# Optimization experiments

Measured on AMD Instinct MI355X. Metric: run time of the kernel, lower is better.

The kernel has to match this reference:

```python
import jax, jax.numpy as jnp
import numpy as np

B, T, D, H, HS = 2, 256, 2048, 32, 64
LORA, DLORA, ST = 32, 64, 66  # maa lora rank, decay lora rank, state rows (2+HS)
EPS = 1e-5


def setup_inputs() -> dict:
    key = jax.random.key(0)
    ks = jax.random.split(key, 24)
    n = lambda k, sh, s=0.02: (jax.random.normal(k, sh, jnp.float32) * s)
    u = lambda k, sh: jax.random.uniform(k, sh, jnp.float32)
    return {
        "x": jax.random.normal(ks[0], (B, T, D), jnp.float32),
        "state": jax.random.normal(ks[1], (B, ST, D), jnp.float32) * 0.1,
        "ln1_w": jnp.ones((D,), jnp.float32),
        "ln1_b": jnp.zeros((D,), jnp.float32),
        "time_maa_x": u(ks[2], (D,)),
        "time_maa_w1": n(ks[3], (D, 5 * LORA)),
        "time_maa_w2": n(ks[4], (5, LORA, D)),
        "time_maa_k": u(ks[5], (D,)),
        "time_maa_w": u(ks[6], (D,)),
        "time_maa_v": u(ks[7], (D,)),
        "time_maa_r": u(ks[8], (D,)),
        "time_maa_g": u(ks[9], (D,)),
        "time_decay": n(ks[10], (D,), 0.5),
        "time_decay_w1": n(ks[11], (D, DLORA)),
        "time_decay_w2": n(ks[12], (DLORA, D)),
        "time_faaaa": n(ks[13], (H, HS, 1), 0.1),
        "receptance_weight": n(ks[14], (D, D)),
        "key_weight": n(ks[15], (D, D)),
        "value_weight": n(ks[16], (D, D)),
        "output_weight": n(ks[17], (D, D)),
        "gate_weight": n(ks[18], (D, D)),
        "lnx_w": jnp.ones((D,), jnp.float32),
        "lnx_b": jnp.zeros((D,), jnp.float32),
        "i": 0,
    }


def reference(x, state, ln1_w, ln1_b, time_maa_x, time_maa_w1, time_maa_w2,
              time_maa_k, time_maa_w, time_maa_v, time_maa_r, time_maa_g,
              time_decay, time_decay_w1, time_decay_w2, time_faaaa,
              receptance_weight, key_weight, value_weight, output_weight,
              gate_weight, lnx_w, lnx_b, i):
    # forward() early-returns time_mixing(ln1(x), state, i)
    mu = x.mean(-1, keepdims=True)
    var = ((x - mu) ** 2).mean(-1, keepdims=True)
    x = (x - mu) * jax.lax.rsqrt(var + EPS) * ln1_w + ln1_b

    i1 = (2 + HS) * i + 1
    # token shift: sx[t] = x[t-1] - x[t], with state row i1 as x[-1]
    sx = jnp.concatenate([state[:, i1][:, None] - x[:, :1], x[:, :-1] - x[:, 1:]], axis=1)

    xxx = x + sx * time_maa_x
    t5 = jnp.tanh(xxx @ time_maa_w1).reshape(B, T, 5, LORA)
    xxx5 = jnp.einsum('btfr,frd->btfd', t5, time_maa_w2)          # [B,T,5,D]
    maa = jnp.stack([time_maa_k, time_maa_w, time_maa_v, time_maa_r, time_maa_g])  # [5,D]
    x5 = x[:, :, None] + sx[:, :, None] * (maa + xxx5)            # [B,T,5,D]

    k = (x5[:, :, 0] @ key_weight.T).reshape(B, T, H, HS)
    w = jnp.exp(-jnp.exp(time_decay + jnp.tanh(x5[:, :, 1] @ time_decay_w1) @ time_decay_w2)).reshape(B, T, H, HS)
    v = (x5[:, :, 2] @ value_weight.T).reshape(B, T, H, HS)
    r = (x5[:, :, 3] @ receptance_weight.T).reshape(B, T, H, HS)
    g = jax.nn.silu(x5[:, :, 4] @ gate_weight.T)                  # [B,T,D]

    kv = jnp.einsum('bthi,bthj->bthij', k, v)                     # [B,T,H,HS,HS]
    prev0 = state[:, i1 + 1:i1 + 1 + HS].reshape(B, H, HS, HS)

    def step(prev, xs):
        kv_t, w_t = xs
        return kv_t + w_t[..., None] * prev, prev  # emit state BEFORE update

    _, state_s = jax.lax.scan(step, prev0,
                              (kv.transpose(1, 0, 2, 3, 4), w.transpose(1, 0, 2, 3)))
    state_s = state_s.transpose(1, 0, 2, 3, 4)                    # [B,T,H,HS,HS]

    wkv = time_faaaa * kv + state_s
    rwkv = jnp.einsum('bthj,bthjd->bthd', r, wkv)                 # [B,T,H,HS]

    # GroupNorm(num_groups=H) over each head's HS channels
    gm = rwkv.mean(-1, keepdims=True)
    gv = ((rwkv - gm) ** 2).mean(-1, keepdims=True)
    normed = (rwkv - gm) * jax.lax.rsqrt(gv + EPS)
    normed = normed * lnx_w.reshape(H, HS) + lnx_b.reshape(H, HS)
    normed = normed.reshape(B, T, D)

    return (normed * g) @ output_weight.T
```

## Files before the change

kernel.cpp:

```cpp
#include <hip/hip_runtime.h>
#include <hip/hip_bf16.h>

typedef unsigned short u16;
typedef __attribute__((ext_vector_type(4))) float f32x4;
typedef __attribute__((ext_vector_type(8))) short short8;
typedef __attribute__((ext_vector_type(4))) short bf16x4;

#define B_ 2
#define T_ 256
#define D_ 2048
#define H_ 32
#define HS_ 64
#define M_ 512
#define ST_ 66
#define EPS_ 1e-5f

__device__ __forceinline__ float bf2f(u16 u) {
    union { unsigned int i; float f; } c; c.i = ((unsigned int)u) << 16; return c.f;
}
__device__ __forceinline__ u16 f2bf(float f) {
    union { unsigned int i; float f; } c; c.f = f;
    unsigned int r = c.i + 0x7fffu + ((c.i >> 16) & 1u);
    return (u16)(r >> 16);
}

__device__ __forceinline__ void gld16(const u16* g, u16* l) {
    __builtin_amdgcn_global_load_lds((const __attribute__((address_space(1))) void*)g,
                                     (__attribute__((address_space(3))) void*)l, 16, 0, 0);
}

__global__ __launch_bounds__(256) void wcvt_kernel(const float* __restrict__ wk, const float* __restrict__ wv,
                                                   const float* __restrict__ wr, const float* __restrict__ wg,
                                                   const float* __restrict__ wo, u16* __restrict__ out)
{
    const int wsel = blockIdx.y;
    const float* in = (wsel == 0) ? wk : (wsel == 1) ? wv : (wsel == 2) ? wr : (wsel == 3) ? wg : wo;
    const size_t e = ((size_t)blockIdx.x * 256 + threadIdx.x) * 8;
    f32x4 a = *(const f32x4*)(in + e);
    f32x4 b = *(const f32x4*)(in + e + 4);
    short8 o;
#pragma unroll
    for (int i = 0; i < 4; i++) { o[i] = (short)f2bf(a[i]); o[i + 4] = (short)f2bf(b[i]); }
    *(short8*)(out + (size_t)wsel * D_ * D_ + e) = o;
}

__global__ __launch_bounds__(256) void ln_kernel(const float* __restrict__ x, const float* __restrict__ w,
                                                 const float* __restrict__ bias, float* __restrict__ xln)
{
    const int row = blockIdx.x;
    const float* xr = x + (size_t)row * D_;
    float* orow = xln + (size_t)row * D_;
    const int t = threadIdx.x;
    f32x4 a0 = *(const f32x4*)(xr + t * 8);
    f32x4 a1 = *(const f32x4*)(xr + t * 8 + 4);
    float s = 0.f, q = 0.f;
#pragma unroll
    for (int i = 0; i < 4; i++) { s += a0[i] + a1[i]; q += a0[i]*a0[i] + a1[i]*a1[i]; }
#pragma unroll
    for (int off = 1; off < 64; off <<= 1) { s += __shfl_xor(s, off, 64); q += __shfl_xor(q, off, 64); }
    __shared__ float ls[4], lq[4];
    const int wid = t >> 6, lane = t & 63;
    if (lane == 0) { ls[wid] = s; lq[wid] = q; }
    __syncthreads();
    s = ls[0] + ls[1] + ls[2] + ls[3];
    q = lq[0] + lq[1] + lq[2] + lq[3];
    const float mu = s * (1.f / D_);
    const float var = q * (1.f / D_) - mu * mu;
    const float rs = rsqrtf(var + EPS_);
#pragma unroll
    for (int i = 0; i < 8; i++) {
        int d = t * 8 + i;
        float f = (i < 4) ? a0[i] : a1[i - 4];
        orow[d] = (f - mu) * rs * w[d] + bias[d];
    }
}

__global__ __launch_bounds__(256) void shift_kernel(const float* __restrict__ xln, const float* __restrict__ state,
                                                    const float* __restrict__ maax, const int* __restrict__ ip,
                                                    float* __restrict__ sx, u16* __restrict__ xxxb)
{
    const size_t gid = (size_t)blockIdx.x * 256 + threadIdx.x;
    const size_t e = gid * 4;
    const int row = (int)(e >> 11);
    const int d = (int)(e & 2047);
    const int tt = row & (T_ - 1);
    const int b = row >> 8;
    const float* prev;
    if (tt == 0) prev = state + ((size_t)b * ST_ + (size_t)(66 * ip[0] + 1)) * D_ + d;
    else         prev = xln + e - D_;
    f32x4 p = *(const f32x4*)prev;
    f32x4 c = *(const f32x4*)(xln + e);
    f32x4 mx = *(const f32x4*)(maax + d);
    f32x4 sv;
    bf16x4 xv;
#pragma unroll
    for (int i = 0; i < 4; i++) { sv[i] = p[i] - c[i]; xv[i] = (short)f2bf(c[i] + sv[i] * mx[i]); }
    *(f32x4*)(sx + e) = sv;
    *(bf16x4*)(xxxb + e) = xv;
}

__global__ __launch_bounds__(256) void txp_kernel(const float* __restrict__ in, u16* __restrict__ out,
                                                  int K, int N)
{
    __shared__ float tile[32][33];
    const int k0 = blockIdx.x * 32, n0 = blockIdx.y * 32;
    const int c = threadIdx.x & 31, r8 = threadIdx.x >> 5;
#pragma unroll
    for (int i = 0; i < 4; i++) {
        int r = r8 + i * 8;
        tile[r][c] = in[(size_t)(k0 + r) * N + (n0 + c)];
    }
    __syncthreads();
#pragma unroll
    for (int i = 0; i < 4; i++) {
        int r = r8 + i * 8;
        out[(size_t)(n0 + r) * K + (k0 + c)] = f2bf(tile[c][r]);
    }
}

template<int NN, bool TANH>
__global__ __launch_bounds__(256) void gsmall_kernel(const u16* __restrict__ A, const u16* __restrict__ Wt,
                                                     float* __restrict__ C, int ldc)
{
    __shared__ u16 As[128 * 32];
    __shared__ u16 Ws[64 * 32];
    const int tid = threadIdx.x;
    const int m0 = blockIdx.y * 128, n0 = blockIdx.x * 64;
    const int lane = tid & 63, wid = tid >> 6;
    const int wm = (wid >> 1) * 64, wn = (wid & 1) * 32;

    f32x4 acc[4][2];
#pragma unroll
    for (int i = 0; i < 4; i++)
#pragma unroll
        for (int j = 0; j < 2; j++) { acc[i][j][0]=0.f; acc[i][j][1]=0.f; acc[i][j][2]=0.f; acc[i][j][3]=0.f; }

    const int rA = tid >> 2;
    const int kA = (tid & 3) * 8;
    const u16* gA0 = A + (size_t)(m0 + rA) * D_ + kA;
    const u16* gA1 = A + (size_t)(m0 + rA + 64) * D_ + kA;
    int wrow = n0 + rA; if (wrow >= NN) wrow = NN - 1;
    const u16* gW = Wt + (size_t)wrow * D_ + kA;
    u16* lA0 = As + tid * 8;
    u16* lA1 = As + (tid + 256) * 8;
    u16* lW  = Ws + tid * 8;
    const u16* pa = As + (size_t)(wm + (lane & 15)) * 32 + (lane >> 4) * 8;
    const u16* pb = Ws + (size_t)(wn + (lane & 15)) * 32 + (lane >> 4) * 8;

    short8 a0 = *(const short8*)gA0;
    short8 a1 = *(const short8*)gA1;
    short8 w0 = *(const short8*)gW;

    for (int kt = 0; kt < D_; kt += 32) {
        const int kt2 = (kt + 32) & (D_ - 1);
        short8 na0 = *(const short8*)(gA0 + kt2);
        short8 na1 = *(const short8*)(gA1 + kt2);
        short8 nw0 = *(const short8*)(gW + kt2);
        __syncthreads();
        *(short8*)lA0 = a0;
        *(short8*)lA1 = a1;
        *(short8*)lW  = w0;
        __syncthreads();
        short8 av[4], bv[2];
#pragma unroll
        for (int mi = 0; mi < 4; mi++) av[mi] = *(const short8*)(pa + mi * 16 * 32);
#pragma unroll
        for (int ni = 0; ni < 2; ni++) bv[ni] = *(const short8*)(pb + ni * 16 * 32);
#pragma unroll
        for (int mi = 0; mi < 4; mi++)
#pragma unroll
            for (int ni = 0; ni < 2; ni++)
                acc[mi][ni] = __builtin_amdgcn_mfma_f32_16x16x32_bf16(av[mi], bv[ni], acc[mi][ni], 0, 0, 0);
        a0 = na0; a1 = na1; w0 = nw0;
    }
    const int cr = wm + (lane >> 4) * 4;
    const int cc = wn + (lane & 15);
#pragma unroll
    for (int mi = 0; mi < 4; mi++)
#pragma unroll
        for (int ni = 0; ni < 2; ni++) {
            const int col = n0 + cc + ni * 16;
            if (col < NN) {
#pragma unroll
                for (int j = 0; j < 4; j++) {
                    float v = acc[mi][ni][j];
                    if (TANH) v = tanhf(v);
                    C[(size_t)(m0 + cr + mi * 16 + j) * ldc + col] = v;
                }
            }
        }
}

__global__ __launch_bounds__(256) void maa2_kernel(const float* __restrict__ t5, const float* __restrict__ w2,
                                                   const float* __restrict__ xln, const float* __restrict__ sxp,
                                                   const float* __restrict__ mk, const float* __restrict__ mw,
                                                   const float* __restrict__ mv, const float* __restrict__ mr,
                                                   const float* __restrict__ mg, u16* __restrict__ x5)
{
    const int gid = blockIdx.x * 256 + threadIdx.x;
    const int d = gid & (D_ - 1);
    const int f = (gid >> 11) % 5;
    const int mg4 = gid / (5 * D_);
    const float* maa = (f == 0) ? mk : (f == 1) ? mw : (f == 2) ? mv : (f == 3) ? mr : mg;
    const float mf = maa[d];
    const float* w2f = w2 + (size_t)f * 32 * D_ + d;
    const float* t5b = t5 + (size_t)mg4 * 4 * 160 + f * 32;
    float a0 = 0, a1 = 0, a2 = 0, a3 = 0;
#pragma unroll 8
    for (int r = 0; r < 32; r++) {
        float wv = w2f[(size_t)r * D_];
        a0 = fmaf(t5b[r], wv, a0);
        a1 = fmaf(t5b[160 + r], wv, a1);
        a2 = fmaf(t5b[320 + r], wv, a2);
        a3 = fmaf(t5b[480 + r], wv, a3);
    }
    const float accs[4] = {a0, a1, a2, a3};
    const size_t m0 = (size_t)mg4 * 4;
#pragma unroll
    for (int mm = 0; mm < 4; mm++) {
        size_t e = (m0 + mm) * D_ + d;
        x5[(size_t)f * M_ * D_ + e] = f2bf(xln[e] + sxp[e] * (mf + accs[mm]));
    }
}

__global__ __launch_bounds__(256) void decay2_kernel(const float* __restrict__ td, const float* __restrict__ dw2,
                                                     const float* __restrict__ tdec, float* __restrict__ wout)
{
    const int gid = blockIdx.x * 256 + threadIdx.x;
    const int d = gid & (D_ - 1);
    const int mg4 = gid >> 11;
    const float* wp = dw2 + d;
    const float* tb = td + (size_t)mg4 * 4 * 64;
    float a0 = 0, a1 = 0, a2 = 0, a3 = 0;
#pragma unroll 8
    for (int r = 0; r < 64; r++) {
        float wv = wp[(size_t)r * D_];
        a0 = fmaf(tb[r], wv, a0);
        a1 = fmaf(tb[64 + r], wv, a1);
        a2 = fmaf(tb[128 + r], wv, a2);
        a3 = fmaf(tb[192 + r], wv, a3);
    }
    const float base = tdec[d];
    const float accs[4] = {a0, a1, a2, a3};
#pragma unroll
    for (int mm = 0; mm < 4; mm++)
        wout[((size_t)mg4 * 4 + mm) * D_ + d] = expf(-expf(base + accs[mm]));
}

__device__ __forceinline__ void gemm2p_body(const u16* __restrict__ A, const u16* __restrict__ Wb,
                                            float* __restrict__ C, int m0, int n0, int k0, int KC)
{
    __shared__ u16 As[2][128 * 64];
    __shared__ u16 Bs[2][64 * 64];
    const int tid = threadIdx.x;
    const int lane = tid & 63;
    const int wvd = tid >> 6;
    const int wm = (wvd >> 1) * 64;
    const int wn = (wvd & 1) * 32;

    f32x4 acc[4][2];
#pragma unroll
    for (int i = 0; i < 4; i++)
#pragma unroll
        for (int j = 0; j < 2; j++) { acc[i][j][0]=0.f; acc[i][j][1]=0.f; acc[i][j][2]=0.f; acc[i][j][3]=0.f; }

    const int srow = tid >> 3;
    const int sw8  = (((tid & 7) ^ (srow & 7)) << 3);
    const u16* Ag = A + (size_t)(m0 + srow) * D_ + k0 + sw8;
    const u16* Wg = Wb + (size_t)(n0 + srow) * D_ + k0 + sw8;
    const int ldst = tid * 8;

    const int rsw = (lane & 7) << 3;
    const int colb = (lane >> 4) * 8;
    const int fr = lane & 15;

#define STAGE_(bb, kt)                                                            \
    {                                                                             \
        _Pragma("unroll")                                                         \
        for (int i = 0; i < 4; i++)                                               \
            gld16(Ag + (size_t)(i * 32) * D_ + (kt), &As[bb][i * 2048 + ldst]);   \
        _Pragma("unroll")                                                         \
        for (int i = 0; i < 2; i++)                                               \
            gld16(Wg + (size_t)(i * 32) * D_ + (kt), &Bs[bb][i * 2048 + ldst]);   \
    }

    STAGE_(0, 0);
    __syncthreads();
    int cur = 0;
    for (int kt = 0; kt < KC; kt += 64) {
        if (kt + 64 < KC) STAGE_(cur ^ 1, kt + 64);
#pragma unroll
        for (int kk = 0; kk < 64; kk += 32) {
            const int c = (kk + colb) ^ rsw;
            short8 av[4], bv[2];
#pragma unroll
            for (int mi = 0; mi < 4; mi++)
                av[mi] = *(const short8*)&As[cur][(wm + mi * 16 + fr) * 64 + c];
#pragma unroll
            for (int ni = 0; ni < 2; ni++)
                bv[ni] = *(const short8*)&Bs[cur][(wn + ni * 16 + fr) * 64 + c];
#pragma unroll
            for (int mi = 0; mi < 4; mi++)
#pragma unroll
                for (int ni = 0; ni < 2; ni++)
                    acc[mi][ni] = __builtin_amdgcn_mfma_f32_16x16x32_bf16(av[mi], bv[ni], acc[mi][ni], 0, 0, 0);
        }
        __syncthreads();
        cur ^= 1;
    }
#undef STAGE_
    const int cr = wm + (lane >> 4) * 4;
    const int cc = wn + fr;
#pragma unroll
    for (int mi = 0; mi < 4; mi++)
#pragma unroll
        for (int ni = 0; ni < 2; ni++)
#pragma unroll
            for (int j = 0; j < 4; j++)
                C[(size_t)(m0 + cr + mi * 16 + j) * D_ + (n0 + cc + ni * 16)] = acc[mi][ni][j];
}

__global__ __launch_bounds__(256) void gemm4g_kernel(const u16* __restrict__ x5, const u16* __restrict__ wcvt,
                                                     float* __restrict__ kvK, float* __restrict__ kvV,
                                                     float* __restrict__ kvR, float* __restrict__ kvG)
{
    const int s = blockIdx.z;
    const u16* A = x5 + (size_t)(s == 0 ? 0 : s + 1) * M_ * D_;
    const u16* W = wcvt + (size_t)s * D_ * D_;
    float* C = (s == 0) ? kvK : (s == 1) ? kvV : (s == 2) ? kvR : kvG;
    gemm2p_body(A, W, C, blockIdx.y * 128, blockIdx.x * 64, 0, D_);
}

__global__ __launch_bounds__(256) void gemm1g_kernel(const u16* __restrict__ y, const u16* __restrict__ wo,
                                                     float* __restrict__ out, float* __restrict__ p0,
                                                     float* __restrict__ p1, float* __restrict__ p2)
{
    const int ks = blockIdx.z;
    float* C = (ks == 0) ? out : (ks == 1) ? p0 : (ks == 2) ? p1 : p2;
    gemm2p_body(y, wo, C, blockIdx.y * 128, blockIdx.x * 64, ks * 512, 512);
}

__global__ __launch_bounds__(256) void add3_kernel(float* __restrict__ dst, const float* __restrict__ s0,
                                                   const float* __restrict__ s1, const float* __restrict__ s2)
{
    const size_t e = ((size_t)blockIdx.x * 256 + threadIdx.x) * 4;
    f32x4 d = *(const f32x4*)(dst + e);
    f32x4 a = *(const f32x4*)(s0 + e);
    f32x4 b = *(const f32x4*)(s1 + e);
    f32x4 c = *(const f32x4*)(s2 + e);
#pragma unroll
    for (int i = 0; i < 4; i++) d[i] += (a[i] + b[i]) + c[i];
    *(f32x4*)(dst + e) = d;
}

#define CH_ 16
__global__ __launch_bounds__(512) void rec_kernel(const float* __restrict__ rB, const float* __restrict__ kB,
                                                  const float* __restrict__ wB, const float* __restrict__ vB,
                                                  const float* __restrict__ fa, const float* __restrict__ state,
                                                  const int* __restrict__ ip, float* __restrict__ rwkv)
{
    const int bh = blockIdx.x;
    const int b = bh >> 5, h = bh & 31;
    const int tid = threadIdx.x;
    const int wv = tid >> 6, lane = tid & 63;
    const int wg = wv >> 2;
    const int jb = lane >> 3, dsub = lane & 7;
    const int jbase = jb * 8;
    const int d0 = wg * 32 + (wv & 3) * 8 + dsub;

    __shared__ float stage[2][4][CH_][64];
    __shared__ float p2[CH_][8][64];
    __shared__ float p1[CH_][8];

    float S[8], faj[8];
    {
        const float* Sp = state + (size_t)b * ST_ * D_ + (size_t)(66 * ip[0] + 2) * D_ + (size_t)h * HS_ * HS_;
#pragma unroll
        for (int jj = 0; jj < 8; jj++) {
            S[jj]   = Sp[(jbase + jj) * 64 + d0];
            faj[jj] = fa[h * 64 + jbase + jj];
        }
    }
    const size_t base = ((size_t)b * T_ * H_ + h) * HS_;
    const int arr = wv & 3;
    const float* mysrc = (arr == 0) ? rB : (arr == 1) ? kB : (arr == 2) ? wB : vB;
    const int ts0 = wg * 8 + (lane >> 4);
    const int sch = (lane & 15) * 4;
    const bool p1w = (wv == 0 && dsub == 0);

    f32x4 pre[2];
#pragma unroll
    for (int p = 0; p < 2; p++)
        pre[p] = *(const f32x4*)(mysrc + base + (size_t)(ts0 + p * 4) * (H_ * HS_) + sch);
#pragma unroll
    for (int p = 0; p < 2; p++)
        *(f32x4*)&stage[0][arr][ts0 + p * 4][sch] = pre[p];
    __syncthreads();

    int cb = 0;
    for (int c = 0; c < T_ / CH_; ++c) {
        const bool more = (c + 1 < T_ / CH_);
        if (more) {
#pragma unroll
            for (int p = 0; p < 2; p++)
                pre[p] = *(const f32x4*)(mysrc + base + (size_t)((c + 1) * CH_ + ts0 + p * 4) * (H_ * HS_) + sch);
        }
        f32x4 r0 = *(const f32x4*)&stage[cb][0][0][jbase];
        f32x4 r1 = *(const f32x4*)&stage[cb][0][0][jbase + 4];
        f32x4 k0 = *(const f32x4*)&stage[cb][1][0][jbase];
        f32x4 k1 = *(const f32x4*)&stage[cb][1][0][jbase + 4];
        f32x4 w0 = *(const f32x4*)&stage[cb][2][0][jbase];
        f32x4 w1 = *(const f32x4*)&stage[cb][2][0][jbase + 4];
        float vd = stage[cb][3][0][d0];
#pragma unroll
        for (int ts = 0; ts < CH_; ++ts) {
            f32x4 nr0 = r0, nr1 = r1, nk0 = k0, nk1 = k1, nw0 = w0, nw1 = w1;
            float nvd = vd;
            if (ts + 1 < CH_) {
                nr0 = *(const f32x4*)&stage[cb][0][ts + 1][jbase];
                nr1 = *(const f32x4*)&stage[cb][0][ts + 1][jbase + 4];
                nk0 = *(const f32x4*)&stage[cb][1][ts + 1][jbase];
                nk1 = *(const f32x4*)&stage[cb][1][ts + 1][jbase + 4];
                nw0 = *(const f32x4*)&stage[cb][2][ts + 1][jbase];
                nw1 = *(const f32x4*)&stage[cb][2][ts + 1][jbase + 4];
                nvd = stage[cb][3][ts + 1][d0];
            }
            float s1 = 0.f, s2 = 0.f;
#pragma unroll
            for (int q = 0; q < 4; q++) {
                s1 = fmaf(r0[q] * faj[q],     k0[q], s1);
                s1 = fmaf(r1[q] * faj[q + 4], k1[q], s1);
                s2 = fmaf(r0[q], S[q],     s2);
                s2 = fmaf(r1[q], S[q + 4], s2);
            }
            p2[ts][jb][d0 ^ (jb << 3)] = s2;
            if (p1w) p1[ts][jb] = s1;
#pragma unroll
            for (int q = 0; q < 4; q++) {
                S[q]     = fmaf(w0[q], S[q],     k0[q] * vd);
                S[q + 4] = fmaf(w1[q], S[q + 4], k1[q] * vd);
            }
            r0 = nr0; r1 = nr1; k0 = nk0; k1 = nk1; w0 = nw0; w1 = nw1; vd = nvd;
        }
        if (more) {
#pragma unroll
            for (int p = 0; p < 2; p++)
                *(f32x4*)&stage[cb ^ 1][arr][ts0 + p * 4][sch] = pre[p];
        }
        __syncthreads();
#pragma unroll
        for (int p = 0; p < 2; p++) {
            const int ts = wv * 2 + p;
            f32x4 p1a = *(const f32x4*)&p1[ts][0];
            f32x4 p1b = *(const f32x4*)&p1[ts][4];
            float s1t = ((p1a[0] + p1a[1]) + (p1a[2] + p1a[3])) +
                        ((p1b[0] + p1b[1]) + (p1b[2] + p1b[3]));
            float s2t = 0.f;
#pragma unroll
            for (int j = 0; j < 8; j++) s2t += p2[ts][j][lane ^ (j << 3)];
            const float vvv = stage[cb][3][ts][lane];
            rwkv[base + (size_t)(c * CH_ + ts) * (H_ * HS_) + lane] = fmaf(vvv, s1t, s2t);
        }
        __syncthreads();
        cb ^= 1;
    }
}

__global__ __launch_bounds__(256) void gn_kernel(const float* __restrict__ rwkv, const float* __restrict__ gpre,
                                                 const float* __restrict__ lnxw, const float* __restrict__ lnxb,
                                                 u16* __restrict__ y)
{
    const int g = blockIdx.x * 4 + (threadIdx.x >> 6);
    const int lane = threadIdx.x & 63;
    const size_t e = (size_t)g * 64 + lane;
    const float val = rwkv[e];
    float s = val, q = val * val;
#pragma unroll
    for (int off = 1; off < 64; off <<= 1) { s += __shfl_xor(s, off, 64); q += __shfl_xor(q, off, 64); }
    const float mu = s * (1.f / 64.f);
    const float var = q * (1.f / 64.f) - mu * mu;
    const float rs = rsqrtf(var + EPS_);
    const int hj = (int)(e & (size_t)(D_ - 1));
    const float nrm = (val - mu) * rs * lnxw[hj] + lnxb[hj];
    const float gp = gpre[e];
    const float gv = gp / (1.f + expf(-gp));
    y[e] = f2bf(nrm * gv);
}

extern "C" void kernel_launch(void* const* d_in, const int* in_sizes, int n_in,
                              void* d_out, int out_size, void* d_ws, size_t ws_size,
                              hipStream_t stream)
{
    const float* x     = (const float*)d_in[0];
    const float* state = (const float*)d_in[1];
    const float* ln1w  = (const float*)d_in[2];
    const float* ln1b  = (const float*)d_in[3];
    const float* maax  = (const float*)d_in[4];
    const float* w1    = (const float*)d_in[5];
    const float* w2    = (const float*)d_in[6];
    const float* maak  = (const float*)d_in[7];
    const float* maaw  = (const float*)d_in[8];
    const float* maav  = (const float*)d_in[9];
    const float* maar  = (const float*)d_in[10];
    const float* maag  = (const float*)d_in[11];
    const float* tdec  = (const float*)d_in[12];
    const float* dw1   = (const float*)d_in[13];
    const float* dw2   = (const float*)d_in[14];
    const float* fa    = (const float*)d_in[15];
    const float* wrec  = (const float*)d_in[16];
    const float* wkey  = (const float*)d_in[17];
    const float* wval  = (const float*)d_in[18];
    const float* wout  = (const float*)d_in[19];
    const float* wgate = (const float*)d_in[20];
    const float* lnxw  = (const float*)d_in[21];
    const float* lnxb  = (const float*)d_in[22];
    const int*   ip    = (const int*)d_in[23];

    char* ws = (char*)d_ws;
    const size_t MD = (size_t)M_ * D_;
    u16*   wcvt = (u16*)  (ws);
    float* xln  = (float*)(ws + ((size_t)40 << 20));
    float* sx   = (float*)(ws + ((size_t)44 << 20));
    u16*   xxxb = (u16*)  (ws + ((size_t)48 << 20));
    u16*   w1t  = (u16*)  (ws + ((size_t)50 << 20));
    u16*   dw1t = (u16*)  (ws + ((size_t)51 << 20));
    float* t5   = (float*)(ws + ((size_t)52 << 20));
    float* td   = (float*)(ws + ((size_t)53 << 20));
    u16*   x5   = (u16*)  (ws + ((size_t)54 << 20));
    float* wdec = (float*)(ws + ((size_t)64 << 20));
    float* kvK  = (float*)(ws + ((size_t)40 << 20));
    float* kvV  = (float*)(ws + ((size_t)44 << 20));
    float* kvR  = (float*)(ws + ((size_t)48 << 20));
    float* kvG  = (float*)(ws + ((size_t)68 << 20));
    float* rwkv = (float*)(ws + ((size_t)72 << 20));
    u16*   y    = (u16*)  (ws + ((size_t)76 << 20));
    float* pp0  = (float*)(ws + ((size_t)54 << 20));
    float* pp1  = (float*)(ws + ((size_t)58 << 20));
    float* pp2  = (float*)(ws + ((size_t)62 << 20));
    float* out  = (float*)d_out;

    hipLaunchKernelGGL(wcvt_kernel,   dim3(2048, 5),  dim3(256), 0, stream, wkey, wval, wrec, wgate, wout, wcvt);
    hipLaunchKernelGGL(ln_kernel,     dim3(512),      dim3(256), 0, stream, x, ln1w, ln1b, xln);
    hipLaunchKernelGGL(shift_kernel,  dim3(1024),     dim3(256), 0, stream, xln, state, maax, ip, sx, xxxb);
    hipLaunchKernelGGL(txp_kernel,    dim3(64, 5),    dim3(256), 0, stream, w1, w1t, D_, 160);
    hipLaunchKernelGGL(txp_kernel,    dim3(64, 2),    dim3(256), 0, stream, dw1, dw1t, D_, 64);
    hipLaunchKernelGGL((gsmall_kernel<160, true>), dim3(3, 4), dim3(256), 0, stream, xxxb, w1t, t5, 160);
    hipLaunchKernelGGL(maa2_kernel,   dim3(5120),     dim3(256), 0, stream, t5, w2, xln, sx, maak, maaw, maav, maar, maag, x5);
    hipLaunchKernelGGL((gsmall_kernel<64, true>),  dim3(1, 4), dim3(256), 0, stream, x5 + MD, dw1t, td, 64);
    hipLaunchKernelGGL(decay2_kernel, dim3(1024),     dim3(256), 0, stream, td, dw2, tdec, wdec);
    hipLaunchKernelGGL(gemm4g_kernel, dim3(32, 4, 4), dim3(256), 0, stream, x5, wcvt, kvK, kvV, kvR, kvG);
    hipLaunchKernelGGL(rec_kernel,    dim3(64),       dim3(512), 0, stream, kvR, kvK, wdec, kvV, fa, state, ip, rwkv);
    hipLaunchKernelGGL(gn_kernel,     dim3(4096),     dim3(256), 0, stream, rwkv, kvG, lnxw, lnxb, y);
    hipLaunchKernelGGL(gemm1g_kernel, dim3(32, 4, 4), dim3(256), 0, stream, y, wcvt + (size_t)4 * D_ * D_, out, pp0, pp1, pp2);
    hipLaunchKernelGGL(add3_kernel,   dim3(1024),     dim3(256), 0, stream, out, pp0, pp1, pp2);

    (void)in_sizes; (void)n_in; (void)out_size; (void)ws_size;
}
```

Baseline: 213.8 us.

## Split WKV recurrence into chunked parallel scan across blocks

Replaces the single sequential recurrence kernel (64 blocks iterating all 256 timesteps) with a three-phase chunked scan. Chunks run in parallel from zero state while recording decay products. A small pass then propagates carry states across chunks, and a final pass adds the carried-state contribution via r·prod(w) times the chunk start state. This exposes 16x more blocks to use the GPU, at the cost of two extra launches and extra global traffic for per-chunk states. Workspace at offset 0 is reused for chunk states, which overlaps the weight-conversion buffer.

```diff
diff --git a/kernel.cpp b/kernel.cpp
--- a/kernel.cpp
+++ b/kernel.cpp
@@ -14,6 +14,8 @@
 #define M_ 512
 #define ST_ 66
 #define EPS_ 1e-5f
+#define NC_ 16
+#define CL_ 16
 
 __device__ __forceinline__ float bf2f(u16 u) {
     union { unsigned int i; float f; } c; c.i = ((unsigned int)u) << 16; return c.f;
@@ -353,14 +355,16 @@
     *(f32x4*)(dst + e) = d;
 }
 
-#define CH_ 16
-__global__ __launch_bounds__(512) void rec_kernel(const float* __restrict__ rB, const float* __restrict__ kB,
-                                                  const float* __restrict__ wB, const float* __restrict__ vB,
-                                                  const float* __restrict__ fa, const float* __restrict__ state,
-                                                  const int* __restrict__ ip, float* __restrict__ rwkv)
-{
-    const int bh = blockIdx.x;
-    const int b = bh >> 5, h = bh & 31;
+__global__ __launch_bounds__(512) void rec1_kernel(const float* __restrict__ rB, const float* __restrict__ kB,
+                                                   const float* __restrict__ wB, const float* __restrict__ vB,
+                                                   const float* __restrict__ fa, float* __restrict__ rwkv,
+                                                   float* __restrict__ CS, float* __restrict__ RP,
+                                                   float* __restrict__ PC)
+{
+    const int bx = blockIdx.x;
+    const int c  = bx & (NC_ - 1);
+    const int bh = bx >> 4;
+    const int h = bh & 31, b = bh >> 5;
     const int tid = threadIdx.x;
     const int wv = tid >> 6, lane = tid & 63;
     const int wg = wv >> 2;
@@ -368,102 +372,159 @@
     const int jbase = jb * 8;
     const int d0 = wg * 32 + (wv & 3) * 8 + dsub;
 
-    __shared__ float stage[2][4][CH_][64];
-    __shared__ float p2[CH_][8][64];
-    __shared__ float p1[CH_][8];
-
-    float S[8], faj[8];
-    {
-        const float* Sp = state + (size_t)b * ST_ * D_ + (size_t)(66 * ip[0] + 2) * D_ + (size_t)h * HS_ * HS_;
-#pragma unroll
-        for (int jj = 0; jj < 8; jj++) {
-            S[jj]   = Sp[(jbase + jj) * 64 + d0];
-            faj[jj] = fa[h * 64 + jbase + jj];
-        }
-    }
+    __shared__ float stage[4][CL_][64];
+    __shared__ float p2[CL_][8][64];
+    __shared__ float p1[CL_][8];
+    __shared__ float rpS[CL_ * 64];
+
+    float S[8], pv[8], faj[8];
+#pragma unroll
+    for (int q = 0; q < 8; q++) { S[q] = 0.f; pv[q] = 1.f; faj[q] = fa[h * 64 + jbase + q]; }
+
     const size_t base = ((size_t)b * T_ * H_ + h) * HS_;
+    const int t0 = c * CL_;
     const int arr = wv & 3;
     const float* mysrc = (arr == 0) ? rB : (arr == 1) ? kB : (arr == 2) ? wB : vB;
     const int ts0 = wg * 8 + (lane >> 4);
     const int sch = (lane & 15) * 4;
     const bool p1w = (wv == 0 && dsub == 0);
 
-    f32x4 pre[2];
-#pragma unroll
-    for (int p = 0; p < 2; p++)
-        pre[p] = *(const f32x4*)(mysrc + base + (size_t)(ts0 + p * 4) * (H_ * HS_) + sch);
-#pragma unroll
-    for (int p = 0; p < 2; p++)
-        *(f32x4*)&stage[0][arr][ts0 + p * 4][sch] = pre[p];
+#pragma unroll
+    for (int p = 0; p < 2; p++) {
+        f32x4 v = *(const f32x4*)(mysrc + base + (size_t)(t0 + ts0 + p * 4) * (H_ * HS_) + sch);
+        *(f32x4*)&stage[arr][ts0 + p * 4][sch] = v;
+    }
     __syncthreads();
 
-    int cb = 0;
-    for (int c = 0; c < T_ / CH_; ++c) {
-        const bool more = (c + 1 < T_ / CH_);
-        if (more) {
-#pragma unroll
-            for (int p = 0; p < 2; p++)
-                pre[p] = *(const f32x4*)(mysrc + base + (size_t)((c + 1) * CH_ + ts0 + p * 4) * (H_ * HS_) + sch);
+    f32x4 r0 = *(const f32x4*)&stage[0][0][jbase];
+    f32x4 r1 = *(const f32x4*)&stage[0][0][jbase + 4];
+    f32x4 k0 = *(const f32x4*)&stage[1][0][jbase];
+    f32x4 k1 = *(const f32x4*)&stage[1][0][jbase + 4];
+    f32x4 w0 = *(const f32x4*)&stage[2][0][jbase];
+    f32x4 w1 = *(const f32x4*)&stage[2][0][jbase + 4];
+    float vd = stage[3][0][d0];
+#pragma unroll
+    for (int ts = 0; ts < CL_; ++ts) {
+        f32x4 nr0 = r0, nr1 = r1, nk0 = k0, nk1 = k1, nw0 = w0, nw1 = w1;
+        float nvd = vd;
+        if (ts + 1 < CL_) {
+            nr0 = *(const f32x4*)&stage[0][ts + 1][jbase];
+            nr1 = *(const f32x4*)&stage[0][ts + 1][jbase + 4];
+            nk0 = *(const f32x4*)&stage[1][ts + 1][jbase];
+            nk1 = *(const f32x4*)&stage[1][ts + 1][jbase + 4];
+            nw0 = *(const f32x4*)&stage[2][ts + 1][jbase];
+            nw1 = *(const f32x4*)&stage[2][ts + 1][jbase + 4];
+            nvd = stage[3][ts + 1][d0];
         }
-        f32x4 r0 = *(const f32x4*)&stage[cb][0][0][jbase];
-        f32x4 r1 = *(const f32x4*)&stage[cb][0][0][jbase + 4];
-        f32x4 k0 = *(const f32x4*)&stage[cb][1][0][jbase];
-        f32x4 k1 = *(const f32x4*)&stage[cb][1][0][jbase + 4];
-        f32x4 w0 = *(const f32x4*)&stage[cb][2][0][jbase];
-        f32x4 w1 = *(const f32x4*)&stage[cb][2][0][jbase + 4];
-        float vd = stage[cb][3][0][d0];
-#pragma unroll
-        for (int ts = 0; ts < CH_; ++ts) {
-            f32x4 nr0 = r0, nr1 = r1, nk0 = k0, nk1 = k1, nw0 = w0, nw1 = w1;
-            float nvd = vd;
-            if (ts + 1 < CH_) {
-                nr0 = *(const f32x4*)&stage[cb][0][ts + 1][jbase];
-                nr1 = *(const f32x4*)&stage[cb][0][ts + 1][jbase + 4];
-                nk0 = *(const f32x4*)&stage[cb][1][ts + 1][jbase];
-                nk1 = *(const f32x4*)&stage[cb][1][ts + 1][jbase + 4];
-                nw0 = *(const f32x4*)&stage[cb][2][ts + 1][jbase];
-                nw1 = *(const f32x4*)&stage[cb][2][ts + 1][jbase + 4];
-                nvd = stage[cb][3][ts + 1][d0];
+        float s1 = 0.f, s2 = 0.f;
+#pragma unroll
+        for (int q = 0; q < 4; q++) {
+            s1 = fmaf(r0[q] * faj[q],     k0[q], s1);
+            s1 = fmaf(r1[q] * faj[q + 4], k1[q], s1);
+            s2 = fmaf(r0[q], S[q],     s2);
+            s2 = fmaf(r1[q], S[q + 4], s2);
+        }
+        p2[ts][jb][d0 ^ (jb << 3)] = s2;
+        if (p1w) {
+            p1[ts][jb] = s1;
+#pragma unroll
+            for (int q = 0; q < 4; q++) {
+                rpS[ts * 64 + jbase + q]     = r0[q] * pv[q];
+                rpS[ts * 64 + jbase + 4 + q] = r1[q] * pv[q + 4];
             }
-            float s1 = 0.f, s2 = 0.f;
-#pragma unroll
-            for (int q = 0; q < 4; q++) {
-                s1 = fmaf(r0[q] * faj[q],     k0[q], s1);
-                s1 = fmaf(r1[q] * faj[q + 4], k1[q], s1);
-                s2 = fmaf(r0[q], S[q],     s2);
-                s2 = fmaf(r1[q], S[q + 4], s2);
-            }
-            p2[ts][jb][d0 ^ (jb << 3)] = s2;
-            if (p1w) p1[ts][jb] = s1;
-#pragma unroll
-            for (int q = 0; q < 4; q++) {
-                S[q]     = fmaf(w0[q], S[q],     k0[q] * vd);
-                S[q + 4] = fmaf(w1[q], S[q + 4], k1[q] * vd);
-            }
-            r0 = nr0; r1 = nr1; k0 = nk0; k1 = nk1; w0 = nw0; w1 = nw1; vd = nvd;
         }
-        if (more) {
-#pragma unroll
-            for (int p = 0; p < 2; p++)
-                *(f32x4*)&stage[cb ^ 1][arr][ts0 + p * 4][sch] = pre[p];
+#pragma unroll
+        for (int q = 0; q < 4; q++) {
+            pv[q]     *= w0[q];
+            pv[q + 4] *= w1[q];
+            S[q]       = fmaf(w0[q], S[q],     k0[q] * vd);
+            S[q + 4]   = fmaf(w1[q], S[q + 4], k1[q] * vd);
         }
-        __syncthreads();
-#pragma unroll
-        for (int p = 0; p < 2; p++) {
-            const int ts = wv * 2 + p;
-            f32x4 p1a = *(const f32x4*)&p1[ts][0];
-            f32x4 p1b = *(const f32x4*)&p1[ts][4];
-            float s1t = ((p1a[0] + p1a[1]) + (p1a[2] + p1a[3])) +
-                        ((p1b[0] + p1b[1]) + (p1b[2] + p1b[3]));
-            float s2t = 0.f;
-#pragma unroll
-            for (int j = 0; j < 8; j++) s2t += p2[ts][j][lane ^ (j << 3)];
-            const float vvv = stage[cb][3][ts][lane];
-            rwkv[base + (size_t)(c * CH_ + ts) * (H_ * HS_) + lane] = fmaf(vvv, s1t, s2t);
-        }
-        __syncthreads();
-        cb ^= 1;
-    }
+        r0 = nr0; r1 = nr1; k0 = nk0; k1 = nk1; w0 = nw0; w1 = nw1; vd = nvd;
+    }
+    __syncthreads();
+#pragma unroll
+    for (int p = 0; p < 2; p++) {
+        const int ts = wv * 2 + p;
+        f32x4 p1a = *(const f32x4*)&p1[ts][0];
+        f32x4 p1b = *(const f32x4*)&p1[ts][4];
+        float s1t = ((p1a[0] + p1a[1]) + (p1a[2] + p1a[3])) +
+                    ((p1b[0] + p1b[1]) + (p1b[2] + p1b[3]));
+        float s2t = 0.f;
+#pragma unroll
+        for (int j = 0; j < 8; j++) s2t += p2[ts][j][lane ^ (j << 3)];
+        const float vvv = stage[3][ts][lane];
+        rwkv[base + (size_t)(t0 + ts) * (H_ * HS_) + lane] = fmaf(vvv, s1t, s2t);
+    }
+    RP[(size_t)bx * (CL_ * 64) + tid]       = rpS[tid];
+    RP[(size_t)bx * (CL_ * 64) + 512 + tid] = rpS[512 + tid];
+#pragma unroll
+    for (int q = 0; q < 8; q++)
+        CS[(size_t)bx * 4096 + (size_t)(jbase + q) * 64 + d0] = S[q];
+    if (p1w) {
+#pragma unroll
+        for (int q = 0; q < 8; q++)
+            PC[(size_t)bx * 64 + jbase + q] = pv[q];
+    }
+}
+
+__global__ __launch_bounds__(512) void rec2_kernel(const float* __restrict__ state, const int* __restrict__ ip,
+                                                   float* __restrict__ CS, const float* __restrict__ PC)
+{
+    const int bh = blockIdx.x;
+    const int b = bh >> 5, h = bh & 31;
+    const int tid = threadIdx.x;
+    const int o = tid * 8;
+    const int jrow = tid >> 3;
+    const float* Sp = state + (size_t)b * ST_ * D_ + (size_t)(66 * ip[0] + 2) * D_ + (size_t)h * HS_ * HS_;
+    f32x4 c0 = *(const f32x4*)(Sp + o);
+    f32x4 c1 = *(const f32x4*)(Sp + o + 4);
+    for (int c = 0; c < NC_; ++c) {
+        float* cs = CS + ((size_t)(bh * NC_ + c)) * 4096 + o;
+        f32x4 l0 = *(const f32x4*)cs;
+        f32x4 l1 = *(const f32x4*)(cs + 4);
+        const float pc = PC[(size_t)(bh * NC_ + c) * 64 + jrow];
+        f32x4 n0, n1;
+#pragma unroll
+        for (int i = 0; i < 4; i++) { n0[i] = fmaf(pc, c0[i], l0[i]); n1[i] = fmaf(pc, c1[i], l1[i]); }
+        *(f32x4*)cs = c0;
+        *(f32x4*)(cs + 4) = c1;
+        c0 = n0; c1 = n1;
+    }
+}
+
+__global__ __launch_bounds__(256) void rec3_kernel(const float* __restrict__ CS, const float* __restrict__ RP,
+                                                   float* __restrict__ rwkv)
+{
+    const int bx = blockIdx.x;
+    const int c  = bx & (NC_ - 1);
+    const int bh = bx >> 4;
+    const int h = bh & 31, b = bh >> 5;
+    const int tid = threadIdx.x;
+    __shared__ float Ss[4096];
+    __shared__ float rp[CL_ * 64];
+#pragma unroll
+    for (int i = 0; i < 4; i++)
+        *(f32x4*)&Ss[tid * 4 + i * 1024] = *(const f32x4*)(CS + (size_t)bx * 4096 + tid * 4 + i * 1024);
+    *(f32x4*)&rp[tid * 4] = *(const f32x4*)(RP + (size_t)bx * (CL_ * 64) + tid * 4);
+    __syncthreads();
+    const int tl = tid >> 4;
+    const int d4 = (tid & 15) * 4;
+    f32x4 acc; acc[0] = acc[1] = acc[2] = acc[3] = 0.f;
+    const float* rpr = &rp[tl * 64];
+#pragma unroll 16
+    for (int j = 0; j < 64; ++j) {
+        const float rv = rpr[j];
+        const f32x4 sv = *(const f32x4*)&Ss[j * 64 + d4];
+#pragma unroll
+        for (int i = 0; i < 4; i++) acc[i] = fmaf(rv, sv[i], acc[i]);
+    }
+    const size_t base = ((size_t)b * T_ * H_ + h) * HS_;
+    float* o = rwkv + base + (size_t)(c * CL_ + tl) * (H_ * HS_) + d4;
+    f32x4 cur = *(const f32x4*)o;
+#pragma unroll
+    for (int i = 0; i < 4; i++) cur[i] += acc[i];
+    *(f32x4*)o = cur;
 }
 
 __global__ __launch_bounds__(256) void gn_kernel(const float* __restrict__ rwkv, const float* __restrict__ gpre,
@@ -534,6 +595,9 @@
     float* kvG  = (float*)(ws + ((size_t)68 << 20));
     float* rwkv = (float*)(ws + ((size_t)72 << 20));
     u16*   y    = (u16*)  (ws + ((size_t)76 << 20));
+    float* CS   = (float*)(ws);
+    float* RP   = (float*)(ws + ((size_t)16 << 20));
+    float* PC   = (float*)(ws + ((size_t)20 << 20));
     float* pp0  = (float*)(ws + ((size_t)54 << 20));
     float* pp1  = (float*)(ws + ((size_t)58 << 20));
     float* pp2  = (float*)(ws + ((size_t)62 << 20));
@@ -549,7 +613,9 @@
     hipLaunchKernelGGL((gsmall_kernel<64, true>),  dim3(1, 4), dim3(256), 0, stream, x5 + MD, dw1t, td, 64);
     hipLaunchKernelGGL(decay2_kernel, dim3(1024),     dim3(256), 0, stream, td, dw2, tdec, wdec);
     hipLaunchKernelGGL(gemm4g_kernel, dim3(32, 4, 4), dim3(256), 0, stream, x5, wcvt, kvK, kvV, kvR, kvG);
-    hipLaunchKernelGGL(rec_kernel,    dim3(64),       dim3(512), 0, stream, kvR, kvK, wdec, kvV, fa, state, ip, rwkv);
+    hipLaunchKernelGGL(rec1_kernel,   dim3(B_ * H_ * NC_), dim3(512), 0, stream, kvR, kvK, wdec, kvV, fa, rwkv, CS, RP, PC);
+    hipLaunchKernelGGL(rec2_kernel,   dim3(B_ * H_),  dim3(512), 0, stream, state, ip, CS, PC);
+    hipLaunchKernelGGL(rec3_kernel,   dim3(B_ * H_ * NC_), dim3(256), 0, stream, CS, RP, rwkv);
     hipLaunchKernelGGL(gn_kernel,     dim3(4096),     dim3(256), 0, stream, rwkv, kvG, lnxw, lnxb, y);
     hipLaunchKernelGGL(gemm1g_kernel, dim3(32, 4, 4), dim3(256), 0, stream, y, wcvt + (size_t)4 * D_ * D_, out, pp0, pp1, pp2);
     hipLaunchKernelGGL(add3_kernel,   dim3(1024),     dim3(256), 0, stream, out, pp0, pp1, pp2);
```

Result: faster. 206.4 us (-3.5%).
